# Kernel optimization log

Hardware: AMD Instinct MI355X
Metric: run time of the kernel (lower is better)

The kernel has to match this reference:

```python
import jax, jax.numpy as jnp
import numpy as np

B_POINTS = 1024   # batch of independent spatial points
NF = 672          # hourly forcing samples (28 days * 24 h)

def setup_inputs() -> dict:
    key = jax.random.key(0)
    k1, k2, k3 = jax.random.split(key, 3)
    # pk ~ [-10, -9] as in the source, with small perturbation
    pk = jnp.array([-10.0, -9.0], jnp.float32) + 0.1 * jax.random.normal(k1, (2,), jnp.float32)
    # wind stress ~ O(0.1) N/m^2
    TAx = 0.1 * jax.random.normal(k2, (B_POINTS, NF), jnp.float32)
    TAy = 0.1 * jax.random.normal(k3, (B_POINTS, NF), jnp.float32)
    fc = jnp.float32(1e-4)  # Coriolis frequency
    return {"pk": pk, "TAx": TAx, "TAy": TAy, "fc": fc,
            "nt": 40320, "dt": 60, "dt_forcing": 3600}

def reference(pk, TAx, TAy, fc, nt, dt, dt_forcing):
    # Slab-ocean 1D model, explicit Euler (difx=True branch of the source):
    #   dU/dt =  fc*V + K0*TAx(t) - K1*U
    #   dV/dt = -fc*U + K0*TAy(t) - K1*V
    # with TAx/TAy linearly interpolated from hourly forcing to the dt grid.
    K = jnp.exp(pk)                       # [2]
    nsub = dt_forcing // dt               # substeps per forcing sample (60)
    nf = TAx.shape[-1]                    # number of forcing samples
    dtf = jnp.float32(dt)

    def step(carry, it):
        U, V = carry                      # [B], [B]
        itf = it // nsub
        aa = (jnp.mod(it, nsub) / nsub).astype(jnp.float32)
        itsup = jnp.where(itf + 1 >= nf, nf - 1, itf + 1)
        tax = (1.0 - aa) * TAx[:, itf] + aa * TAx[:, itsup]
        tay = (1.0 - aa) * TAy[:, itf] + aa * TAy[:, itsup]
        Un = U + dtf * ( fc * V + K[0] * tax - K[1] * U)
        Vn = V + dtf * (-fc * U + K[0] * tay - K[1] * V)
        return (Un, Vn), Un

    B = TAx.shape[0]
    U0 = jnp.zeros((B,), jnp.float32)
    _, Us = jax.lax.scan(step, (U0, U0), jnp.arange(nt, dtype=jnp.int32))
    return Us  # [nt, B] zonal velocity saved after each Euler step
```

## Files before the change

kernel.cpp:

```cpp
#include <hip/hip_runtime.h>


#define NT    40320
#define BPTS  1024
#define NF    672
#define NSUB  60
#define CH    60
#define NCH   (NT / CH)
#define CPL   11
#define PPT   4
#define WPB   4

typedef float vf4 __attribute__((ext_vector_type(4)));

__device__ __forceinline__ void coefs(const float* pk, const float* fcp, const int* dtp,
                                      float& ar, float& ai, float& bs) {
    float dtf = (float)dtp[0];
    float K0 = expf(pk[0]);
    float K1 = expf(pk[1]);
    ar = 1.0f - dtf * K1;
    ai = -dtf * fcp[0];
    bs = dtf * K0;
}

__global__ __launch_bounds__(256)
void slab_scan(const float* __restrict__ pk,
               const float* __restrict__ TAx,
               const float* __restrict__ TAy,
               const float* __restrict__ fcp,
               const int* __restrict__ dtp,
               float2* __restrict__ ZS) {
    const int wave = threadIdx.x >> 6;
    const int l    = threadIdx.x & 63;
    const int p    = blockIdx.x * WPB + wave;

    __shared__ float sx[WPB][NF];
    __shared__ float sy[WPB][NF];
    const float* rx = TAx + (size_t)p * NF;
    const float* ry = TAy + (size_t)p * NF;
    for (int t = l; t < NF; t += 64) { sx[wave][t] = rx[t]; sy[wave][t] = ry[t]; }
    __syncthreads();

    float ar, ai, bs;
    coefs(pk, fcp, dtp, ar, ai, bs);

    float g1r = 0.f, g1i = 0.f, g2r = 0.f, g2i = 0.f;
    float pr = 1.f, pi = 0.f;
    for (int m = 0; m < NSUB; ++m) {
        g1r += pr; g1i += pi;
        float w = (float)(NSUB - 1 - m) * (1.0f / NSUB);
        g2r = fmaf(w, pr, g2r); g2i = fmaf(w, pi, g2i);
        float nr = pr * ar - pi * ai;
        float ni = pr * ai + pi * ar;
        pr = nr; pi = ni;
    }
    const float Ar  = pr,        Ai  = pi;
    const float cAr = g1r - g2r, cAi = g1i - g2i;
    const float cBr = g2r,       cBi = g2i;

    float qr[CPL], qi[CPL];
    float zr = 0.f, zi = 0.f;
#pragma unroll
    for (int i = 0; i < CPL; ++i) {
        qr[i] = zr; qi[i] = zi;
        const int k = l * CPL + i;
        float sr = 0.f, si = 0.f;
        if (k < NCH) {
            const int f1 = (k + 1 < NF) ? k + 1 : NF - 1;
            float wr0 = bs * sx[wave][k],  wi0 = bs * sy[wave][k];
            float wr1 = bs * sx[wave][f1], wi1 = bs * sy[wave][f1];
            sr = cAr * wr0 - cAi * wi0 + cBr * wr1 - cBi * wi1;
            si = cAr * wi0 + cAi * wr0 + cBr * wi1 + cBi * wr1;
        }
        float nr = Ar * zr - Ai * zi + sr;
        float ni = Ar * zi + Ai * zr + si;
        zr = nr; zi = ni;
    }

    float Pr = 1.f, Pi = 0.f;
    for (int m = 0; m < CPL; ++m) {
        float nr = Pr * Ar - Pi * Ai;
        float ni = Pr * Ai + Pi * Ar;
        Pr = nr; Pi = ni;
    }
    float Vr = zr, Vi = zi;

#pragma unroll
    for (int d = 1; d < 64; d <<= 1) {
        float pr2 = __shfl_up(Pr, d), pi2 = __shfl_up(Pi, d);
        float vr2 = __shfl_up(Vr, d), vi2 = __shfl_up(Vi, d);
        if (l >= d) {
            float nVr = Pr * vr2 - Pi * vi2 + Vr;
            float nVi = Pr * vi2 + Pi * vr2 + Vi;
            float nPr = Pr * pr2 - Pi * pi2;
            float nPi = Pr * pi2 + Pi * pr2;
            Pr = nPr; Pi = nPi; Vr = nVr; Vi = nVi;
        }
    }
    float Er = __shfl_up(Vr, 1), Ei = __shfl_up(Vi, 1);
    if (l == 0) { Er = 0.f; Ei = 0.f; }

#pragma unroll
    for (int i = 0; i < CPL; ++i) {
        const int k = l * CPL + i;
        if (k < NCH)
            ZS[(size_t)k * BPTS + p] = make_float2(Er + qr[i], Ei + qi[i]);
        float nr = Ar * Er - Ai * Ei;
        float ni = Ar * Ei + Ai * Er;
        Er = nr; Ei = ni;
    }
}

__global__ __launch_bounds__(256)
void slab_write(const float* __restrict__ pk,
                const float* __restrict__ TAx,
                const float* __restrict__ TAy,
                const float* __restrict__ fcp,
                const int* __restrict__ dtp,
                const float2* __restrict__ ZS,
                float* __restrict__ out) {
    const int k  = blockIdx.x;
    const int p0 = threadIdx.x * PPT;

    const int f0 = k;
    const int f1 = (k + 1 < NF) ? k + 1 : NF - 1;

    float zr[PPT], zi[PPT];
    float x0[PPT], x1[PPT], y0[PPT], y1[PPT];
#pragma unroll
    for (int j = 0; j < PPT; ++j) {
        float2 z = ZS[(size_t)k * BPTS + p0 + j];
        zr[j] = z.x; zi[j] = z.y;
        const float* rx = TAx + (size_t)(p0 + j) * NF;
        const float* ry = TAy + (size_t)(p0 + j) * NF;
        x0[j] = rx[f0]; x1[j] = rx[f1];
        y0[j] = ry[f0]; y1[j] = ry[f1];
    }

    float ar, ai, bs;
    coefs(pk, fcp, dtp, ar, ai, bs);

    float bx[PPT], by[PPT], dbx[PPT], dby[PPT];
#pragma unroll
    for (int j = 0; j < PPT; ++j) {
        bx[j]  = bs * x0[j];
        by[j]  = bs * y0[j];
        dbx[j] = bs * (x1[j] - x0[j]) * (1.0f / NSUB);
        dby[j] = bs * (y1[j] - y0[j]) * (1.0f / NSUB);
    }

    float* orow = out + (size_t)k * CH * BPTS + p0;

#pragma unroll 10
    for (int s = 0; s < CH; ++s) {
#pragma unroll
        for (int j = 0; j < PPT; ++j) {
            float ur = fmaf(ar, zr[j], fmaf(-ai, zi[j], bx[j]));
            float vi = fmaf(ar, zi[j], fmaf( ai, zr[j], by[j]));
            zr[j] = ur; zi[j] = vi;
            bx[j] += dbx[j]; by[j] += dby[j];
        }
        vf4 v; v.x = zr[0]; v.y = zr[1]; v.z = zr[2]; v.w = zr[3];
        __builtin_nontemporal_store(v, (vf4*)orow);
        orow += BPTS;
    }
}

extern "C" void kernel_launch(void* const* d_in, const int* in_sizes, int n_in,
                              void* d_out, int out_size, void* d_ws, size_t ws_size,
                              hipStream_t stream) {
    const float* pk  = (const float*)d_in[0];
    const float* TAx = (const float*)d_in[1];
    const float* TAy = (const float*)d_in[2];
    const float* fcp = (const float*)d_in[3];
    const int*   dtp = (const int*)d_in[5];
    float* out = (float*)d_out;

    float2* ZS = (float2*)d_ws;

    slab_scan <<<BPTS / WPB, 256, 0, stream>>>(pk, TAx, TAy, fcp, dtp, ZS);
    slab_write<<<NCH,        256, 0, stream>>>(pk, TAx, TAy, fcp, dtp, ZS, out);
}
```

Before: 54.54 us.

## Fuse scan and write kernels into one cooperative kernel with grid sync

Merges the two-kernel pipeline into a single cooperative launch of 256 blocks. Each block first runs the per-point chunk scan, then a grid-wide barrier separates it from the write phase, in which each block handles up to three chunks. This removes the second kernel launch and the gap between kernels. In exchange it adds grid-sync overhead and gives the write phase fewer blocks (256 instead of 672), which may lower memory-level parallelism for the large output store.

```diff
diff --git a/kernel.cpp b/kernel.cpp
--- a/kernel.cpp
+++ b/kernel.cpp
@@ -1,4 +1,5 @@
 #include <hip/hip_runtime.h>
+#include <hip/hip_cooperative_groups.h>
 
 
 #define NT    40320
@@ -10,8 +11,12 @@
 #define CPL   11
 #define PPT   4
 #define WPB   4
+#define GRID  256
+#define CPB   3
 
 typedef float vf4 __attribute__((ext_vector_type(4)));
+
+namespace cg = cooperative_groups;
 
 __device__ __forceinline__ void coefs(const float* pk, const float* fcp, const int* dtp,
                                       float& ar, float& ai, float& bs) {
@@ -24,145 +29,145 @@
 }
 
 __global__ __launch_bounds__(256)
-void slab_scan(const float* __restrict__ pk,
-               const float* __restrict__ TAx,
-               const float* __restrict__ TAy,
-               const float* __restrict__ fcp,
-               const int* __restrict__ dtp,
-               float2* __restrict__ ZS) {
+void slab_all(const float* __restrict__ pk,
+              const float* __restrict__ TAx,
+              const float* __restrict__ TAy,
+              const float* __restrict__ fcp,
+              const int* __restrict__ dtp,
+              float2* __restrict__ ZS,
+              float* __restrict__ out) {
     const int wave = threadIdx.x >> 6;
     const int l    = threadIdx.x & 63;
-    const int p    = blockIdx.x * WPB + wave;
-
-    __shared__ float sx[WPB][NF];
-    __shared__ float sy[WPB][NF];
-    const float* rx = TAx + (size_t)p * NF;
-    const float* ry = TAy + (size_t)p * NF;
-    for (int t = l; t < NF; t += 64) { sx[wave][t] = rx[t]; sy[wave][t] = ry[t]; }
-    __syncthreads();
 
     float ar, ai, bs;
     coefs(pk, fcp, dtp, ar, ai, bs);
 
-    float g1r = 0.f, g1i = 0.f, g2r = 0.f, g2i = 0.f;
-    float pr = 1.f, pi = 0.f;
-    for (int m = 0; m < NSUB; ++m) {
-        g1r += pr; g1i += pi;
-        float w = (float)(NSUB - 1 - m) * (1.0f / NSUB);
-        g2r = fmaf(w, pr, g2r); g2i = fmaf(w, pi, g2i);
-        float nr = pr * ar - pi * ai;
-        float ni = pr * ai + pi * ar;
-        pr = nr; pi = ni;
-    }
-    const float Ar  = pr,        Ai  = pi;
-    const float cAr = g1r - g2r, cAi = g1i - g2i;
-    const float cBr = g2r,       cBi = g2i;
+    {
+        const int p = blockIdx.x * WPB + wave;
 
-    float qr[CPL], qi[CPL];
-    float zr = 0.f, zi = 0.f;
+        __shared__ float sx[WPB][NF];
+        __shared__ float sy[WPB][NF];
+        const float* rx = TAx + (size_t)p * NF;
+        const float* ry = TAy + (size_t)p * NF;
+        for (int t = l; t < NF; t += 64) { sx[wave][t] = rx[t]; sy[wave][t] = ry[t]; }
+        __syncthreads();
+
+        float g1r = 0.f, g1i = 0.f, g2r = 0.f, g2i = 0.f;
+        float pr = 1.f, pi = 0.f;
+        for (int m = 0; m < NSUB; ++m) {
+            g1r += pr; g1i += pi;
+            float w = (float)(NSUB - 1 - m) * (1.0f / NSUB);
+            g2r = fmaf(w, pr, g2r); g2i = fmaf(w, pi, g2i);
+            float nr = pr * ar - pi * ai;
+            float ni = pr * ai + pi * ar;
+            pr = nr; pi = ni;
+        }
+        const float Ar  = pr,        Ai  = pi;
+        const float cAr = g1r - g2r, cAi = g1i - g2i;
+        const float cBr = g2r,       cBi = g2i;
+
+        float qr[CPL], qi[CPL];
+        float zr = 0.f, zi = 0.f;
 #pragma unroll
-    for (int i = 0; i < CPL; ++i) {
-        qr[i] = zr; qi[i] = zi;
-        const int k = l * CPL + i;
-        float sr = 0.f, si = 0.f;
-        if (k < NCH) {
-            const int f1 = (k + 1 < NF) ? k + 1 : NF - 1;
-            float wr0 = bs * sx[wave][k],  wi0 = bs * sy[wave][k];
-            float wr1 = bs * sx[wave][f1], wi1 = bs * sy[wave][f1];
-            sr = cAr * wr0 - cAi * wi0 + cBr * wr1 - cBi * wi1;
-            si = cAr * wi0 + cAi * wr0 + cBr * wi1 + cBi * wr1;
+        for (int i = 0; i < CPL; ++i) {
+            qr[i] = zr; qi[i] = zi;
+            const int k = l * CPL + i;
+            float sr = 0.f, si = 0.f;
+            if (k < NCH) {
+                const int f1 = (k + 1 < NF) ? k + 1 : NF - 1;
+                float wr0 = bs * sx[wave][k],  wi0 = bs * sy[wave][k];
+                float wr1 = bs * sx[wave][f1], wi1 = bs * sy[wave][f1];
+                sr = cAr * wr0 - cAi * wi0 + cBr * wr1 - cBi * wi1;
+                si = cAr * wi0 + cAi * wr0 + cBr * wi1 + cBi * wr1;
+            }
+            float nr = Ar * zr - Ai * zi + sr;
+            float ni = Ar * zi + Ai * zr + si;
+            zr = nr; zi = ni;
         }
-        float nr = Ar * zr - Ai * zi + sr;
-        float ni = Ar * zi + Ai * zr + si;
-        zr = nr; zi = ni;
+
+        float Pr = 1.f, Pi = 0.f;
+        for (int m = 0; m < CPL; ++m) {
+            float nr = Pr * Ar - Pi * Ai;
+            float ni = Pr * Ai + Pi * Ar;
+            Pr = nr; Pi = ni;
+        }
+        float Vr = zr, Vi = zi;
+
+#pragma unroll
+        for (int d = 1; d < 64; d <<= 1) {
+            float pr2 = __shfl_up(Pr, d), pi2 = __shfl_up(Pi, d);
+            float vr2 = __shfl_up(Vr, d), vi2 = __shfl_up(Vi, d);
+            if (l >= d) {
+                float nVr = Pr * vr2 - Pi * vi2 + Vr;
+                float nVi = Pr * vi2 + Pi * vr2 + Vi;
+                float nPr = Pr * pr2 - Pi * pi2;
+                float nPi = Pr * pi2 + Pi * pr2;
+                Pr = nPr; Pi = nPi; Vr = nVr; Vi = nVi;
+            }
+        }
+        float Er = __shfl_up(Vr, 1), Ei = __shfl_up(Vi, 1);
+        if (l == 0) { Er = 0.f; Ei = 0.f; }
+
+#pragma unroll
+        for (int i = 0; i < CPL; ++i) {
+            const int k = l * CPL + i;
+            if (k < NCH)
+                ZS[(size_t)k * BPTS + p] = make_float2(Er + qr[i], Ei + qi[i]);
+            float nr = Ar * Er - Ai * Ei;
+            float ni = Ar * Ei + Ai * Er;
+            Er = nr; Ei = ni;
+        }
     }
 
-    float Pr = 1.f, Pi = 0.f;
-    for (int m = 0; m < CPL; ++m) {
-        float nr = Pr * Ar - Pi * Ai;
-        float ni = Pr * Ai + Pi * Ar;
-        Pr = nr; Pi = ni;
-    }
-    float Vr = zr, Vi = zi;
+    __threadfence();
+    cg::this_grid().sync();
+    __threadfence();
 
-#pragma unroll
-    for (int d = 1; d < 64; d <<= 1) {
-        float pr2 = __shfl_up(Pr, d), pi2 = __shfl_up(Pi, d);
-        float vr2 = __shfl_up(Vr, d), vi2 = __shfl_up(Vi, d);
-        if (l >= d) {
-            float nVr = Pr * vr2 - Pi * vi2 + Vr;
-            float nVi = Pr * vi2 + Pi * vr2 + Vi;
-            float nPr = Pr * pr2 - Pi * pi2;
-            float nPi = Pr * pi2 + Pi * pr2;
-            Pr = nPr; Pi = nPi; Vr = nVr; Vi = nVi;
-        }
-    }
-    float Er = __shfl_up(Vr, 1), Ei = __shfl_up(Vi, 1);
-    if (l == 0) { Er = 0.f; Ei = 0.f; }
-
-#pragma unroll
-    for (int i = 0; i < CPL; ++i) {
-        const int k = l * CPL + i;
-        if (k < NCH)
-            ZS[(size_t)k * BPTS + p] = make_float2(Er + qr[i], Ei + qi[i]);
-        float nr = Ar * Er - Ai * Ei;
-        float ni = Ar * Ei + Ai * Er;
-        Er = nr; Ei = ni;
-    }
-}
-
-__global__ __launch_bounds__(256)
-void slab_write(const float* __restrict__ pk,
-                const float* __restrict__ TAx,
-                const float* __restrict__ TAy,
-                const float* __restrict__ fcp,
-                const int* __restrict__ dtp,
-                const float2* __restrict__ ZS,
-                float* __restrict__ out) {
-    const int k  = blockIdx.x;
     const int p0 = threadIdx.x * PPT;
 
-    const int f0 = k;
-    const int f1 = (k + 1 < NF) ? k + 1 : NF - 1;
+    for (int r = 0; r < CPB; ++r) {
+        const int k = blockIdx.x + GRID * r;
+        if (k >= NCH) break;
 
-    float zr[PPT], zi[PPT];
-    float x0[PPT], x1[PPT], y0[PPT], y1[PPT];
+        const int f0 = k;
+        const int f1 = (k + 1 < NF) ? k + 1 : NF - 1;
+
+        float zr[PPT], zi[PPT];
+        float x0[PPT], x1[PPT], y0[PPT], y1[PPT];
 #pragma unroll
-    for (int j = 0; j < PPT; ++j) {
-        float2 z = ZS[(size_t)k * BPTS + p0 + j];
-        zr[j] = z.x; zi[j] = z.y;
-        const float* rx = TAx + (size_t)(p0 + j) * NF;
-        const float* ry = TAy + (size_t)(p0 + j) * NF;
-        x0[j] = rx[f0]; x1[j] = rx[f1];
-        y0[j] = ry[f0]; y1[j] = ry[f1];
-    }
+        for (int j = 0; j < PPT; ++j) {
+            float2 z = ZS[(size_t)k * BPTS + p0 + j];
+            zr[j] = z.x; zi[j] = z.y;
+            const float* rx = TAx + (size_t)(p0 + j) * NF;
+            const float* ry = TAy + (size_t)(p0 + j) * NF;
+            x0[j] = rx[f0]; x1[j] = rx[f1];
+            y0[j] = ry[f0]; y1[j] = ry[f1];
+        }
 
-    float ar, ai, bs;
-    coefs(pk, fcp, dtp, ar, ai, bs);
+        float bx[PPT], by[PPT], dbx[PPT], dby[PPT];
+#pragma unroll
+        for (int j = 0; j < PPT; ++j) {
+            bx[j]  = bs * x0[j];
+            by[j]  = bs * y0[j];
+            dbx[j] = bs * (x1[j] - x0[j]) * (1.0f / NSUB);
+            dby[j] = bs * (y1[j] - y0[j]) * (1.0f / NSUB);
+        }
 
-    float bx[PPT], by[PPT], dbx[PPT], dby[PPT];
-#pragma unroll
-    for (int j = 0; j < PPT; ++j) {
-        bx[j]  = bs * x0[j];
-        by[j]  = bs * y0[j];
-        dbx[j] = bs * (x1[j] - x0[j]) * (1.0f / NSUB);
-        dby[j] = bs * (y1[j] - y0[j]) * (1.0f / NSUB);
-    }
-
-    float* orow = out + (size_t)k * CH * BPTS + p0;
+        float* orow = out + (size_t)k * CH * BPTS + p0;
 
 #pragma unroll 10
-    for (int s = 0; s < CH; ++s) {
+        for (int s = 0; s < CH; ++s) {
 #pragma unroll
-        for (int j = 0; j < PPT; ++j) {
-            float ur = fmaf(ar, zr[j], fmaf(-ai, zi[j], bx[j]));
-            float vi = fmaf(ar, zi[j], fmaf( ai, zr[j], by[j]));
-            zr[j] = ur; zi[j] = vi;
-            bx[j] += dbx[j]; by[j] += dby[j];
+            for (int j = 0; j < PPT; ++j) {
+                float ur = fmaf(ar, zr[j], fmaf(-ai, zi[j], bx[j]));
+                float vi = fmaf(ar, zi[j], fmaf( ai, zr[j], by[j]));
+                zr[j] = ur; zi[j] = vi;
+                bx[j] += dbx[j]; by[j] += dby[j];
+            }
+            vf4 v; v.x = zr[0]; v.y = zr[1]; v.z = zr[2]; v.w = zr[3];
+            __builtin_nontemporal_store(v, (vf4*)orow);
+            orow += BPTS;
         }
-        vf4 v; v.x = zr[0]; v.y = zr[1]; v.z = zr[2]; v.w = zr[3];
-        __builtin_nontemporal_store(v, (vf4*)orow);
-        orow += BPTS;
     }
 }
 
@@ -178,6 +183,8 @@
 
     float2* ZS = (float2*)d_ws;
 
-    slab_scan <<<BPTS / WPB, 256, 0, stream>>>(pk, TAx, TAy, fcp, dtp, ZS);
-    slab_write<<<NCH,        256, 0, stream>>>(pk, TAx, TAy, fcp, dtp, ZS, out);
+    void* args[] = { (void*)&pk, (void*)&TAx, (void*)&TAy, (void*)&fcp,
+                     (void*)&dtp, (void*)&ZS, (void*)&out };
+    hipLaunchCooperativeKernel((void*)slab_all, dim3(GRID), dim3(256),
+                               args, 0, stream);
 }
```

Result: slower. 145.8 us (+167.3%).
